# Kernel optimization log

Measured on AMD Instinct MI355X. Metric: run time of the kernel, lower is better.

Reference implementation:

```python
import jax, jax.numpy as jnp
import numpy as np

EPS = 1e-10

def setup_inputs() -> dict:
    key = jax.random.key(0)
    k1, k2, k3 = jax.random.split(key, 3)
    B, R, S, C = 4, 4096, 96, 32
    colors = jax.random.uniform(k1, (B, R, S, C), dtype=jnp.float32)
    densities = jax.random.normal(k2, (B, R, S, 1), dtype=jnp.float32)
    # depths: sorted increasing along the sample axis, in a plausible near/far range
    depths = jnp.sort(jax.random.uniform(k3, (B, R, S, 1), dtype=jnp.float32) * 1.8 + 0.8, axis=2)
    return {"colors": colors, "densities": densities, "depths": depths}

def reference(colors, densities, depths):
    # clamp_mode == 'softplus', white_back == False, foreground-only path
    deltas = depths[:, :, 1:] - depths[:, :, :-1]                      # [B,R,S-1,1]
    colors_mid = (colors[:, :, :-1] + colors[:, :, 1:]) * 0.5          # [B,R,S-1,C]
    densities_mid = (densities[:, :, :-1] + densities[:, :, 1:]) * 0.5
    depths_mid = (depths[:, :, :-1] + depths[:, :, 1:]) * 0.5

    densities_mid = jax.nn.softplus(densities_mid - 1.0)
    density_delta = densities_mid * deltas
    alpha = 1.0 - jnp.exp(-density_delta)                              # [B,R,S-1,1]

    ones = jnp.ones_like(alpha[:, :, :1])
    alpha_shifted = jnp.concatenate([ones, 1.0 - alpha + EPS], axis=-2)  # [B,R,S,1]
    transmittance = jnp.cumprod(alpha_shifted, axis=-2)                # per-ray scan
    weights = alpha * transmittance[:, :, :-1]                         # [B,R,S-1,1]
    weight_bg = transmittance[:, :, -1][..., None]                     # [B,R,1,1]

    composite_rgb = jnp.sum(weights * colors_mid, axis=-2)             # [B,R,C]
    weight_total = jnp.sum(weights, axis=2)                            # [B,R,1]
    composite_depth = jnp.sum(weights * depths_mid, axis=-2) / weight_total
    composite_depth = jnp.where(jnp.isnan(composite_depth), jnp.inf, composite_depth)
    composite_depth = jnp.clip(composite_depth, jnp.min(depths), jnp.max(depths))

    composite_rgb = composite_rgb * 2.0 - 1.0
    return composite_rgb, composite_depth, weights, alpha, weight_bg
```

## Files before the change

### kernel.cpp

```cpp
#include <hip/hip_runtime.h>
#include <math.h>

#define NS 96
#define SM1 95
#define NC 32
#define REPS 1e-10f

__global__ __launch_bounds__(256) void raymarch_fused(
    const float* __restrict__ colors,
    const float* __restrict__ densities,
    const float* __restrict__ depths,
    float* __restrict__ out_rgb,
    float* __restrict__ out_depth,
    float* __restrict__ out_w,
    float* __restrict__ out_alpha,
    float* __restrict__ out_wbg,
    float* __restrict__ ws_d0,
    float* __restrict__ ws_d1)
{
    const int ray  = blockIdx.x * 4 + (threadIdx.x >> 6);
    const int lane = threadIdx.x & 63;

    const float4* col4 = (const float4*)(colors + (size_t)ray * NS * NC);
    float4 v[12];
    #pragma unroll
    for (int k = 0; k < 12; ++k) {
        v[k] = col4[lane + 64 * k];
    }

    const float* dep = depths + (size_t)ray * NS;
    const float* den = densities + (size_t)ray * NS;

    const int i1 = 64 + lane;
    float dep0 = dep[lane];
    float den0 = den[lane];
    float dep1 = (i1 < NS) ? dep[i1] : 0.0f;
    float den1 = (i1 < NS) ? den[i1] : 0.0f;

    float dn0 = __shfl(dep0, (lane + 1) & 63);
    float en0 = __shfl(den0, (lane + 1) & 63);
    float d64 = __shfl(dep1, 0);
    float e64 = __shfl(den1, 0);
    if (lane == 63) { dn0 = d64; en0 = e64; }
    float dn1 = __shfl(dep1, (lane + 1) & 63);
    float en1 = __shfl(den1, (lane + 1) & 63);

    float dm0  = 0.5f * (den0 + en0) - 1.0f;
    float sp0  = fmaxf(dm0, 0.0f) + __logf(1.0f + __expf(-fabsf(dm0)));
    float a0   = 1.0f - __expf(-sp0 * (dn0 - dep0));
    float mid0 = 0.5f * (dep0 + dn0);

    float a1 = 0.0f, mid1 = 0.0f;
    if (lane < 31) {
        float dm1 = 0.5f * (den1 + en1) - 1.0f;
        float sp1 = fmaxf(dm1, 0.0f) + __logf(1.0f + __expf(-fabsf(dm1)));
        a1   = 1.0f - __expf(-sp1 * (dn1 - dep1));
        mid1 = 0.5f * (dep1 + dn1);
    }

    float oma0 = 1.0f - a0 + REPS;
    float oma1 = (lane < 31) ? (1.0f - a1 + REPS) : 1.0f;

    float x = oma0;
    #pragma unroll
    for (int off = 1; off < 64; off <<= 1) {
        float vv = __shfl_up(x, off);
        if (lane >= off) x *= vv;
    }
    float total0 = __shfl(x, 63);

    float y = oma1;
    #pragma unroll
    for (int off = 1; off < 64; off <<= 1) {
        float vv = __shfl_up(y, off);
        if (lane >= off) y *= vv;
    }

    float xs = __shfl_up(x, 1);
    float T0 = (lane == 0) ? 1.0f : xs;
    float w0 = a0 * T0;
    float ys = __shfl_up(y, 1);
    float T1 = ((lane == 0) ? 1.0f : ys) * total0;
    float w1 = a1 * T1;

    float wbg = __shfl(y, 30) * total0;

    float w0p = __shfl_up(w0, 1);
    float c0  = 0.5f * (((lane == 0) ? 0.0f : w0p) + w0);
    float w1p = __shfl_up(w1, 1);
    float w63 = __shfl(w0, 63);
    float c1  = 0.5f * (((lane == 0) ? w63 : w1p) + w1);

    float wsum = w0 + w1;
    float dsum = w0 * mid0 + ((lane < 31) ? w1 * mid1 : 0.0f);
    #pragma unroll
    for (int off = 32; off > 0; off >>= 1) {
        wsum += __shfl_xor(wsum, off);
        dsum += __shfl_xor(dsum, off);
    }

    const size_t b95 = (size_t)ray * SM1;
    out_alpha[b95 + lane] = a0;
    out_w[b95 + lane]     = w0;
    if (lane < 31) {
        out_alpha[b95 + 64 + lane] = a1;
        out_w[b95 + 64 + lane]     = w1;
    }
    float dlast = __shfl(dep1, 31);
    if (lane == 0) {
        out_wbg[ray] = wbg;
        float cd = dsum / wsum;
        if (cd != cd) cd = __builtin_inff();
        out_depth[ray] = cd;
        ws_d0[ray] = dep0;
        ws_d1[ray] = dlast;
    }

    const int srow = lane >> 3;
    float4 acc = {0.0f, 0.0f, 0.0f, 0.0f};
    #pragma unroll
    for (int k = 0; k < 8; ++k) {
        float c = __shfl(c0, srow + 8 * k);
        acc.x = fmaf(c, v[k].x, acc.x);
        acc.y = fmaf(c, v[k].y, acc.y);
        acc.z = fmaf(c, v[k].z, acc.z);
        acc.w = fmaf(c, v[k].w, acc.w);
    }
    #pragma unroll
    for (int k = 8; k < 12; ++k) {
        float c = __shfl(c1, srow + 8 * (k - 8));
        acc.x = fmaf(c, v[k].x, acc.x);
        acc.y = fmaf(c, v[k].y, acc.y);
        acc.z = fmaf(c, v[k].z, acc.z);
        acc.w = fmaf(c, v[k].w, acc.w);
    }

    #pragma unroll
    for (int m = 8; m < 64; m <<= 1) {
        acc.x += __shfl_xor(acc.x, m);
        acc.y += __shfl_xor(acc.y, m);
        acc.z += __shfl_xor(acc.z, m);
        acc.w += __shfl_xor(acc.w, m);
    }

    if (lane < 8) {
        float4 o;
        o.x = 2.0f * acc.x - 1.0f;
        o.y = 2.0f * acc.y - 1.0f;
        o.z = 2.0f * acc.z - 1.0f;
        o.w = 2.0f * acc.w - 1.0f;
        ((float4*)(out_rgb + (size_t)ray * NC))[lane] = o;
    }
}

__global__ __launch_bounds__(256) void raymarch_finalize(
    const float* __restrict__ ws_d0,
    const float* __restrict__ ws_d1,
    float* __restrict__ out_depth,
    int rays)
{
    __shared__ float s_mn[256];
    __shared__ float s_mx[256];
    const int tid = threadIdx.x;

    float mn = __builtin_inff();
    float mx = -__builtin_inff();
    for (int r = tid; r < rays; r += 256) {
        mn = fminf(mn, ws_d0[r]);
        mx = fmaxf(mx, ws_d1[r]);
    }
    s_mn[tid] = mn;
    s_mx[tid] = mx;
    __syncthreads();
    for (int off = 128; off > 0; off >>= 1) {
        if (tid < off) {
            s_mn[tid] = fminf(s_mn[tid], s_mn[tid + off]);
            s_mx[tid] = fmaxf(s_mx[tid], s_mx[tid + off]);
        }
        __syncthreads();
    }
    const float dmin = s_mn[0];
    const float dmax = s_mx[0];

    const int r = blockIdx.x * 256 + tid;
    if (r < rays) {
        float cd = out_depth[r];
        cd = fminf(fmaxf(cd, dmin), dmax);
        out_depth[r] = cd;
    }
}

extern "C" void kernel_launch(void* const* d_in, const int* in_sizes, int n_in,
                              void* d_out, int out_size, void* d_ws, size_t ws_size,
                              hipStream_t stream) {
    const float* colors    = (const float*)d_in[0];
    const float* densities = (const float*)d_in[1];
    const float* depths    = (const float*)d_in[2];

    const int rays = in_sizes[2] / NS;

    float* out = (float*)d_out;
    float* out_rgb   = out;
    float* out_depth = out_rgb + (size_t)rays * NC;
    float* out_w     = out_depth + rays;
    float* out_alpha = out_w + (size_t)rays * SM1;
    float* out_wbg   = out_alpha + (size_t)rays * SM1;

    float* ws    = (float*)d_ws;
    float* ws_d0 = ws;
    float* ws_d1 = ws + rays;

    raymarch_fused<<<rays / 4, 256, 0, stream>>>(
        colors, densities, depths,
        out_rgb, out_depth, out_w, out_alpha, out_wbg, ws_d0, ws_d1);

    raymarch_finalize<<<(rays + 255) / 256, 256, 0, stream>>>(
        ws_d0, ws_d1, out_depth, rays);
}
```

Measured before the change: 303.2 us.

## Use DPP scans and direct neighbor loads, compute depth bounds from inputs

Replaces the shuffle-based product scans, shifts and part of the color reduction with DPP row operations and readlane. Neighbor depth and density values are now loaded directly from memory instead of exchanged through cross-lane shuffles. The finalize kernel drops the workspace arrays and reads first and last depths straight from the input, reducing them with wave shuffles instead of a shared-memory tree. This is meant to cut LDS-permute latency and workspace traffic. In exchange, the finalize pass now does strided loads over every ray in each block.

```diff
diff --git a/kernel.cpp b/kernel.cpp
--- a/kernel.cpp
+++ b/kernel.cpp
@@ -5,6 +5,32 @@
 #define SM1 95
 #define NC 32
 #define REPS 1e-10f
+
+#define DPP_ROW_SHR(n)  (0x110 + (n))
+#define DPP_ROW_ROR(n)  (0x120 + (n))
+#define DPP_WF_SR1      0x138
+#define DPP_ROW_BCAST15 0x142
+#define DPP_ROW_BCAST31 0x143
+
+template <int CTRL, int ROW_MASK>
+__device__ __forceinline__ float dppf(float x, float oldv) {
+    return __int_as_float(__builtin_amdgcn_update_dpp(
+        __float_as_int(oldv), __float_as_int(x), CTRL, ROW_MASK, 0xF, false));
+}
+
+__device__ __forceinline__ float rdlanef(float x, int lane) {
+    return __int_as_float(__builtin_amdgcn_readlane(__float_as_int(x), lane));
+}
+
+__device__ __forceinline__ float scan_prod64(float x) {
+    x *= dppf<DPP_ROW_SHR(1), 0xF>(x, 1.0f);
+    x *= dppf<DPP_ROW_SHR(2), 0xF>(x, 1.0f);
+    x *= dppf<DPP_ROW_SHR(4), 0xF>(x, 1.0f);
+    x *= dppf<DPP_ROW_SHR(8), 0xF>(x, 1.0f);
+    x *= dppf<DPP_ROW_BCAST15, 0xA>(x, 1.0f);
+    x *= dppf<DPP_ROW_BCAST31, 0xC>(x, 1.0f);
+    return x;
+}
 
 __global__ __launch_bounds__(256) void raymarch_fused(
     const float* __restrict__ colors,
@@ -14,36 +40,33 @@
     float* __restrict__ out_depth,
     float* __restrict__ out_w,
     float* __restrict__ out_alpha,
-    float* __restrict__ out_wbg,
-    float* __restrict__ ws_d0,
-    float* __restrict__ ws_d1)
+    float* __restrict__ out_wbg)
 {
     const int ray  = blockIdx.x * 4 + (threadIdx.x >> 6);
     const int lane = threadIdx.x & 63;
 
+    const float* dep = depths + (size_t)ray * NS;
+    const float* den = densities + (size_t)ray * NS;
+
+    const bool hi = (lane < 31);
+    float dep0 = dep[lane];
+    float den0 = den[lane];
+    float dn0  = dep[lane + 1];
+    float en0  = den[lane + 1];
+    float dep1 = 0.0f, den1 = 0.0f, dn1 = 0.0f, en1 = 0.0f;
+    if (hi) {
+        dep1 = dep[64 + lane];
+        den1 = den[64 + lane];
+        dn1  = dep[65 + lane];
+        en1  = den[65 + lane];
+    }
+
     const float4* col4 = (const float4*)(colors + (size_t)ray * NS * NC);
     float4 v[12];
     #pragma unroll
     for (int k = 0; k < 12; ++k) {
         v[k] = col4[lane + 64 * k];
     }
-
-    const float* dep = depths + (size_t)ray * NS;
-    const float* den = densities + (size_t)ray * NS;
-
-    const int i1 = 64 + lane;
-    float dep0 = dep[lane];
-    float den0 = den[lane];
-    float dep1 = (i1 < NS) ? dep[i1] : 0.0f;
-    float den1 = (i1 < NS) ? den[i1] : 0.0f;
-
-    float dn0 = __shfl(dep0, (lane + 1) & 63);
-    float en0 = __shfl(den0, (lane + 1) & 63);
-    float d64 = __shfl(dep1, 0);
-    float e64 = __shfl(den1, 0);
-    if (lane == 63) { dn0 = d64; en0 = e64; }
-    float dn1 = __shfl(dep1, (lane + 1) & 63);
-    float en1 = __shfl(den1, (lane + 1) & 63);
 
     float dm0  = 0.5f * (den0 + en0) - 1.0f;
     float sp0  = fmaxf(dm0, 0.0f) + __logf(1.0f + __expf(-fabsf(dm0)));
@@ -51,7 +74,7 @@
     float mid0 = 0.5f * (dep0 + dn0);
 
     float a1 = 0.0f, mid1 = 0.0f;
-    if (lane < 31) {
+    if (hi) {
         float dm1 = 0.5f * (den1 + en1) - 1.0f;
         float sp1 = fmaxf(dm1, 0.0f) + __logf(1.0f + __expf(-fabsf(dm1)));
         a1   = 1.0f - __expf(-sp1 * (dn1 - dep1));
@@ -59,40 +82,25 @@
     }
 
     float oma0 = 1.0f - a0 + REPS;
-    float oma1 = (lane < 31) ? (1.0f - a1 + REPS) : 1.0f;
-
-    float x = oma0;
-    #pragma unroll
-    for (int off = 1; off < 64; off <<= 1) {
-        float vv = __shfl_up(x, off);
-        if (lane >= off) x *= vv;
-    }
-    float total0 = __shfl(x, 63);
-
-    float y = oma1;
-    #pragma unroll
-    for (int off = 1; off < 64; off <<= 1) {
-        float vv = __shfl_up(y, off);
-        if (lane >= off) y *= vv;
-    }
-
-    float xs = __shfl_up(x, 1);
-    float T0 = (lane == 0) ? 1.0f : xs;
+    float oma1 = hi ? (1.0f - a1 + REPS) : 1.0f;
+
+    float x = scan_prod64(oma0);
+    float y = scan_prod64(oma1);
+    float total0 = rdlanef(x, 63);
+
+    float T0 = dppf<DPP_WF_SR1, 0xF>(x, 1.0f);
     float w0 = a0 * T0;
-    float ys = __shfl_up(y, 1);
-    float T1 = ((lane == 0) ? 1.0f : ys) * total0;
+    float T1 = dppf<DPP_WF_SR1, 0xF>(y, 1.0f) * total0;
     float w1 = a1 * T1;
 
-    float wbg = __shfl(y, 30) * total0;
-
-    float w0p = __shfl_up(w0, 1);
-    float c0  = 0.5f * (((lane == 0) ? 0.0f : w0p) + w0);
-    float w1p = __shfl_up(w1, 1);
-    float w63 = __shfl(w0, 63);
-    float c1  = 0.5f * (((lane == 0) ? w63 : w1p) + w1);
+    float wbg = rdlanef(y, 30) * total0;
+
+    float w63 = rdlanef(w0, 63);
+    float c0 = 0.5f * (dppf<DPP_WF_SR1, 0xF>(w0, 0.0f) + w0);
+    float c1 = 0.5f * (dppf<DPP_WF_SR1, 0xF>(w1, w63) + w1);
 
     float wsum = w0 + w1;
-    float dsum = w0 * mid0 + ((lane < 31) ? w1 * mid1 : 0.0f);
+    float dsum = fmaf(w0, mid0, w1 * mid1);
     #pragma unroll
     for (int off = 32; off > 0; off >>= 1) {
         wsum += __shfl_xor(wsum, off);
@@ -102,18 +110,15 @@
     const size_t b95 = (size_t)ray * SM1;
     out_alpha[b95 + lane] = a0;
     out_w[b95 + lane]     = w0;
-    if (lane < 31) {
+    if (hi) {
         out_alpha[b95 + 64 + lane] = a1;
         out_w[b95 + 64 + lane]     = w1;
     }
-    float dlast = __shfl(dep1, 31);
     if (lane == 0) {
         out_wbg[ray] = wbg;
         float cd = dsum / wsum;
         if (cd != cd) cd = __builtin_inff();
         out_depth[ray] = cd;
-        ws_d0[ray] = dep0;
-        ws_d1[ray] = dlast;
     }
 
     const int srow = lane >> 3;
@@ -135,8 +140,12 @@
         acc.w = fmaf(c, v[k].w, acc.w);
     }
 
-    #pragma unroll
-    for (int m = 8; m < 64; m <<= 1) {
+    acc.x += dppf<DPP_ROW_ROR(8), 0xF>(acc.x, 0.0f);
+    acc.y += dppf<DPP_ROW_ROR(8), 0xF>(acc.y, 0.0f);
+    acc.z += dppf<DPP_ROW_ROR(8), 0xF>(acc.z, 0.0f);
+    acc.w += dppf<DPP_ROW_ROR(8), 0xF>(acc.w, 0.0f);
+    #pragma unroll
+    for (int m = 16; m < 64; m <<= 1) {
         acc.x += __shfl_xor(acc.x, m);
         acc.y += __shfl_xor(acc.y, m);
         acc.z += __shfl_xor(acc.z, m);
@@ -154,45 +163,45 @@
 }
 
 __global__ __launch_bounds__(256) void raymarch_finalize(
-    const float* __restrict__ ws_d0,
-    const float* __restrict__ ws_d1,
+    const float* __restrict__ depths,
     float* __restrict__ out_depth,
     int rays)
 {
-    __shared__ float s_mn[256];
-    __shared__ float s_mx[256];
     const int tid = threadIdx.x;
-
     float mn = __builtin_inff();
     float mx = -__builtin_inff();
     for (int r = tid; r < rays; r += 256) {
-        mn = fminf(mn, ws_d0[r]);
-        mx = fmaxf(mx, ws_d1[r]);
-    }
-    s_mn[tid] = mn;
-    s_mx[tid] = mx;
+        const float* dp = depths + (size_t)r * NS;
+        mn = fminf(mn, dp[0]);
+        mx = fmaxf(mx, dp[SM1]);
+    }
+    #pragma unroll
+    for (int off = 1; off < 64; off <<= 1) {
+        mn = fminf(mn, __shfl_xor(mn, off));
+        mx = fmaxf(mx, __shfl_xor(mx, off));
+    }
+    __shared__ float s_mn[4];
+    __shared__ float s_mx[4];
+    if ((tid & 63) == 0) {
+        s_mn[tid >> 6] = mn;
+        s_mx[tid >> 6] = mx;
+    }
     __syncthreads();
-    for (int off = 128; off > 0; off >>= 1) {
-        if (tid < off) {
-            s_mn[tid] = fminf(s_mn[tid], s_mn[tid + off]);
-            s_mx[tid] = fmaxf(s_mx[tid], s_mx[tid + off]);
-        }
-        __syncthreads();
-    }
-    const float dmin = s_mn[0];
-    const float dmax = s_mx[0];
+    const float dmin = fminf(fminf(s_mn[0], s_mn[1]), fminf(s_mn[2], s_mn[3]));
+    const float dmax = fmaxf(fmaxf(s_mx[0], s_mx[1]), fmaxf(s_mx[2], s_mx[3]));
 
     const int r = blockIdx.x * 256 + tid;
     if (r < rays) {
         float cd = out_depth[r];
-        cd = fminf(fmaxf(cd, dmin), dmax);
-        out_depth[r] = cd;
+        out_depth[r] = fminf(fmaxf(cd, dmin), dmax);
     }
 }
 
 extern "C" void kernel_launch(void* const* d_in, const int* in_sizes, int n_in,
                               void* d_out, int out_size, void* d_ws, size_t ws_size,
                               hipStream_t stream) {
+    (void)d_ws; (void)ws_size; (void)n_in; (void)out_size;
+
     const float* colors    = (const float*)d_in[0];
     const float* densities = (const float*)d_in[1];
     const float* depths    = (const float*)d_in[2];
@@ -206,14 +215,10 @@
     float* out_alpha = out_w + (size_t)rays * SM1;
     float* out_wbg   = out_alpha + (size_t)rays * SM1;
 
-    float* ws    = (float*)d_ws;
-    float* ws_d0 = ws;
-    float* ws_d1 = ws + rays;
-
     raymarch_fused<<<rays / 4, 256, 0, stream>>>(
         colors, densities, depths,
-        out_rgb, out_depth, out_w, out_alpha, out_wbg, ws_d0, ws_d1);
+        out_rgb, out_depth, out_w, out_alpha, out_wbg);
 
     raymarch_finalize<<<(rays + 255) / 256, 256, 0, stream>>>(
-        ws_d0, ws_d1, out_depth, rays);
-}
+        depths, out_depth, rays);
+}
```

Result: slower. 317.4 us (+4.7%).
